# Optimization experiments

Measured on AMD Instinct MI355X. Metric: run time of the kernel, lower is better.

Reference implementation:

```python
import jax, jax.numpy as jnp
import numpy as np

B, H, N, D = 64, 12, 196, 768  # ViT-B/16 @ 224: 196 patch tokens + 1 CLS


def setup_inputs() -> dict:
    key = jax.random.key(0)
    k1, k2, k3 = jax.random.split(key, 3)
    student_tokens = jax.random.normal(k1, (B, N, D), dtype=jnp.float32)
    teacher_tokens = jax.random.normal(k2, (B, N, D), dtype=jnp.float32)
    teacher_attn = jax.random.uniform(k3, (B, H, N + 1, N + 1), dtype=jnp.float32)
    return {
        "student_tokens": student_tokens,
        "teacher_tokens": teacher_tokens,
        "teacher_attn": teacher_attn,
    }


def reference(student_tokens, teacher_tokens, teacher_attn):
    s = student_tokens.astype(jnp.float32)
    t = teacher_tokens.astype(jnp.float32)
    # CLS->patch attention, averaged over heads: [B, N]
    w = teacher_attn[:, :, 0, 1:].mean(axis=1)
    w = w / (w.sum(axis=-1, keepdims=True) + 1e-8)
    s = w[..., None] * s
    t = w[..., None] * t
    # center over token dim
    s_c = s - s.mean(axis=1, keepdims=True)
    t_c = t - t.mean(axis=1, keepdims=True)
    tr_s = jnp.sum(s_c * s_c, axis=(1, 2))  # [B]
    tr_t = jnp.sum(t_c * t_c, axis=(1, 2))  # [B]
    # cross-covariance: [B, D, D]
    cross = jnp.einsum("bnd,bne->bde", s_c, t_c)
    # nuclear norm = sum of singular values
    nuclear = jnp.linalg.svd(cross, compute_uv=False).sum(axis=-1)  # [B]
    loss = jnp.maximum(tr_s + tr_t - 2.0 * nuclear, 0.0).mean()
    return loss
```

## Files before the change

### kernel.cpp

```cpp
#include <hip/hip_runtime.h>
#include <hip/hip_bf16.h>
#include <math.h>

#define NTOK 196
#define NDIM 768
#define NB 64
#define NH 12
#define NA 197
#define MAT (NTOK * NTOK)
#define ATTN_HW (NA * NA)
#define POLAR_ITERS 15

#define PADC 208
#define NTILE 13
#define POLAR_LDS_BYTES (2 * NTOK * PADC * 2)

#define GCH 64
#define GPLANE (208 * GCH)
#define GRAM_LDS_BYTES (2 * GPLANE * 2)

#define FCH 64
#define FA_ROWS 208
#define FB_ROWS 112
#define FAPLANE (FA_ROWS * FCH)
#define FBPLANE (FB_ROWS * FCH)
#define FMF_LDS_BYTES ((2 * FAPLANE + 2 * FBPLANE) * 2)

#define HCH 64
#define HPLANE (208 * HCH)
#define H_LDS_BYTES (2 * HPLANE * 2)
#define NS_SCR_BYTES (8 * 16 * 17 * 4)
#define NS_LDS_BYTES (FMF_LDS_BYTES + NS_SCR_BYTES)

#define POW_LD 197
#define POW_F_WORDS (NTOK * POW_LD)
#define POW_LDS_BYTES ((POW_F_WORDS + 2 * NTOK + 256) * 4)

#define PTLD 208
#define TRI_WORDS 19306
#define CHOL2_PT_WORDS (16 * PTLD)
#define CHOL2_TRI_OFF CHOL2_PT_WORDS
#define CHOL2_ROWOFF_OFF (CHOL2_TRI_OFF + TRI_WORDS)
#define CHOL2_PV_OFF 22832
#define CHOL2_LDS_BYTES ((CHOL2_PV_OFF + 32) * 4)

typedef __attribute__((ext_vector_type(8))) short short8;
typedef __attribute__((ext_vector_type(4))) short short4_t;
typedef __attribute__((ext_vector_type(4))) float f32x4;

__device__ inline short8 s8zero() { short8 z = {0,0,0,0,0,0,0,0}; return z; }

__device__ inline short f2bf(float f) {
  union { float f; unsigned u; } v; v.f = f;
  unsigned u = v.u;
  u += 0x7fffu + ((u >> 16) & 1u);
  return (short)(u >> 16);
}
__device__ inline float bf2f(short s) {
  union { unsigned u; float f; } v;
  v.u = ((unsigned)(unsigned short)s) << 16;
  return v.f;
}

__global__ void k_w(const float* __restrict__ attn, float* __restrict__ wbuf) {
  int b = blockIdx.x;
  int tid = threadIdx.x;
  __shared__ float red[256];
  float w0 = 0.f;
  if (tid < NTOK) {
    size_t base = (size_t)b * NH * ATTN_HW + 1 + tid;
    #pragma unroll
    for (int h = 0; h < NH; ++h) w0 += attn[base + (size_t)h * ATTN_HW];
    w0 *= (1.f / NH);
  }
  red[tid] = (tid < NTOK) ? w0 : 0.f;
  __syncthreads();
  for (int s = 128; s > 0; s >>= 1) { if (tid < s) red[tid] += red[tid + s]; __syncthreads(); }
  float S = red[0];
  if (tid < NTOK) wbuf[b * NTOK + tid] = w0 / (S + 1e-8f);
}

__global__ __launch_bounds__(512, 1) void k_gram_mfma(
    const float* __restrict__ s, const float* __restrict__ t,
    const float* __restrict__ wbuf, float* __restrict__ Gbuf) {
  extern __shared__ short gsm[];
  short* bhp = gsm;
  short* blp = gsm + GPLANE;
  __shared__ float wsh[NTOK];
  int slot = blockIdx.x, b = slot >> 1, src = slot & 1;
  const float* X = (src ? t : s) + (size_t)b * NTOK * NDIM;
  int tid = threadIdx.x;
  int wave = tid >> 6, ln15 = tid & 15, quad = (tid >> 4) & 3;

  if (tid < NTOK) wsh[tid] = wbuf[b * NTOK + tid];
  for (int i = tid; i < 768; i += 512) {
    int p = i / 384, o = i - p * 384;
    ((int*)(gsm + p * GPLANE + 196 * GCH))[o] = 0;
  }
  __syncthreads();

  f32x4 zz = {0.f, 0.f, 0.f, 0.f};
  f32x4 acc[12];
  #pragma unroll
  for (int j = 0; j < 12; ++j) acc[j] = zz;

  for (int c = 0; c < NDIM / GCH; ++c) {
    int kc = c * GCH;
    for (int gi = tid; gi < NTOK * 8; gi += 512) {
      int r = gi >> 3, g = gi & 7;
      const float* sp = X + (size_t)r * NDIM + kc + g * 8;
      float4 f0 = *(const float4*)(sp);
      float4 f1 = *(const float4*)(sp + 4);
      float wv = wsh[r];
      float vs[8] = {f0.x, f0.y, f0.z, f0.w, f1.x, f1.y, f1.z, f1.w};
      short8 hv, lv;
      #pragma unroll
      for (int e = 0; e < 8; ++e) {
        float y = wv * vs[e];
        short hb = f2bf(y);
        hv[e] = hb;
        lv[e] = f2bf(y - bf2f(hb));
      }
      int pg = (g ^ (r & 7)) * 8;
      *(short8*)(bhp + r * GCH + pg) = hv;
      *(short8*)(blp + r * GCH + pg) = lv;
    }
    __syncthreads();
    #pragma unroll
    for (int j = 0; j < 12; ++j) {
      int T = wave + 8 * j;
      if (T < 91) {
        int ti = (int)((sqrtf(8.f * T + 1.f) - 1.f) * 0.5f);
        if ((ti + 1) * (ti + 2) / 2 <= T) ++ti;
        if (ti * (ti + 1) / 2 > T) --ti;
        int tj = T - ti * (ti + 1) / 2;
        int ra = ti * 16 + ln15, rb = tj * 16 + ln15;
        #pragma unroll
        for (int ks = 0; ks < 2; ++ks) {
          int gb0 = ks * 4 + quad;
          int ga = (gb0 ^ (ra & 7)) * 8, gb = (gb0 ^ (rb & 7)) * 8;
          short8 ah = *(const short8*)(bhp + ra * GCH + ga);
          short8 al = *(const short8*)(blp + ra * GCH + ga);
          short8 bhf = *(const short8*)(bhp + rb * GCH + gb);
          short8 blf = *(const short8*)(blp + rb * GCH + gb);
          acc[j] = __builtin_amdgcn_mfma_f32_16x16x32_bf16(ah, bhf, acc[j], 0, 0, 0);
          acc[j] = __builtin_amdgcn_mfma_f32_16x16x32_bf16(ah, blf, acc[j], 0, 0, 0);
          acc[j] = __builtin_amdgcn_mfma_f32_16x16x32_bf16(al, bhf, acc[j], 0, 0, 0);
        }
      }
    }
    __syncthreads();
  }

  float* G = Gbuf + (size_t)slot * MAT;
  #pragma unroll
  for (int j = 0; j < 12; ++j) {
    int T = wave + 8 * j;
    if (T < 91) {
      int ti = (int)((sqrtf(8.f * T + 1.f) - 1.f) * 0.5f);
      if ((ti + 1) * (ti + 2) / 2 <= T) ++ti;
      if (ti * (ti + 1) / 2 > T) --ti;
      int tj = T - ti * (ti + 1) / 2;
      int col = tj * 16 + ln15;
      #pragma unroll
      for (int r = 0; r < 4; ++r) {
        int row = ti * 16 + quad * 4 + r;
        if (row < NTOK && col < NTOK) {
          G[row * NTOK + col] = acc[j][r];
          if (ti != tj) G[col * NTOK + row] = acc[j][r];
        }
      }
    }
  }
}

__global__ void k_center(float* __restrict__ Gbuf, float* __restrict__ trPb) {
  int slot = blockIdx.x;
  float* A = Gbuf + (size_t)slot * MAT;
  __shared__ float r[NTOK];
  __shared__ float red[256];
  __shared__ float gsh, dsh;
  int tid = threadIdx.x;
  float acc = 0.f;
  if (tid < NTOK) {
    for (int m = 0; m < NTOK; ++m) acc += A[m * NTOK + tid];
    r[tid] = acc * (1.f / NTOK);
  }
  red[tid] = (tid < NTOK) ? acc * (1.f / NTOK) : 0.f;
  __syncthreads();
  for (int s = 128; s > 0; s >>= 1) { if (tid < s) red[tid] += red[tid + s]; __syncthreads(); }
  float g = red[0] * (1.f / NTOK);
  float tv = (tid < NTOK) ? (A[tid * NTOK + tid] - 2.f * r[tid] + g) : 0.f;
  __syncthreads();
  red[tid] = tv;
  __syncthreads();
  for (int s = 128; s > 0; s >>= 1) { if (tid < s) red[tid] += red[tid + s]; __syncthreads(); }
  if (tid == 0) {
    float tr = red[0];
    trPb[slot] = tr;
    gsh = g;
    dsh = 1e-4f * fmaxf(tr, 0.f) * (1.f / NTOK);
  }
  __syncthreads();
  float gg = gsh, dd = dsh;
  for (int idx = tid; idx < MAT; idx += 256) {
    int n = idx / NTOK, m = idx - n * NTOK;
    float v = A[idx] - r[n] - r[m] + gg;
    if (n == m) v += dd;
    A[idx] = v;
  }
}

__global__ __launch_bounds__(256, 1) void k_chol_panel(float* __restrict__ Gbuf,
                                                       int transposeOut) {
  extern __shared__ float smf[];
  float* Pt = smf;
  float* tri = smf + CHOL2_TRI_OFF;
  int* rowoff = (int*)(smf + CHOL2_ROWOFF_OFF);
  float* pvb = smf + CHOL2_PV_OFF;
  int slot = blockIdx.x;
  float* A = Gbuf + (size_t)slot * MAT;
  int tid = threadIdx.x;
  if (tid < NTOK) rowoff[tid] = tid * (tid + 1) / 2;
  __syncthreads();
  for (int idx = tid; idx < MAT; idx += 256) {
    int i = idx / NTOK, j = idx - i * NTOK;
    if (j <= i) tri[rowoff[i] + j] = A[idx];
  }
  __syncthreads();

  for (int k0 = 0; k0 < NTOK; k0 += 16) {
    int nb = (NTOK - k0 < 16) ? (NTOK - k0) : 16;
    int t = tid;
    int i = k0 + t;
    bool hasrow = (t < NTOK - k0);
    int ro = hasrow ? rowoff[i] : 0;

    float a[16];
    #pragma unroll
    for (int jj = 0; jj < 16; ++jj) a[jj] = 0.f;
    if (hasrow) {
      #pragma unroll
      for (int jj = 0; jj < 16; ++jj)
        if (jj < nb && k0 + jj <= i) a[jj] = tri[ro + k0 + jj];
    }

    #pragma unroll
    for (int jj = 0; jj < 16; ++jj) {
      bool cv = (jj < nb);
      if (cv && hasrow && t >= jj && t < nb) pvb[((jj & 1) << 4) + t] = a[jj];
      __syncthreads();
      if (cv && hasrow && t >= jj) {
        const float* pv = pvb + ((jj & 1) << 4);
        f32x4 p0 = *(const f32x4*)(pv);
        f32x4 p1 = *(const f32x4*)(pv + 4);
        f32x4 p2 = *(const f32x4*)(pv + 8);
        f32x4 p3 = *(const f32x4*)(pv + 12);
        float pvj = (jj < 4) ? p0[jj & 3] : (jj < 8) ? p1[jj & 3]
                   : (jj < 12) ? p2[jj & 3] : p3[jj & 3];
        float sq = sqrtf(fmaxf(pvj, 1e-20f));
        float pivinv = 1.f / sq;
        float v = a[jj] * pivinv;
        a[jj] = v;
        #pragma unroll
        for (int m = 0; m < 16; ++m) {
          if (m > jj) {
            float pvm = (m < 4) ? p0[m & 3] : (m < 8) ? p1[m & 3]
                       : (m < 12) ? p2[m & 3] : p3[m & 3];
            if (m < nb) a[m] -= v * (pvm * pivinv);
          }
        }
      }
    }

    if (hasrow) {
      #pragma unroll
      for (int jj = 0; jj < 16; ++jj)
        if (jj < nb && k0 + jj <= i) tri[ro + k0 + jj] = a[jj];
      if (t >= nb) {
        #pragma unroll
        for (int jj = 0; jj < 16; ++jj)
          if (jj < nb) Pt[jj * PTLD + i] = a[jj];
      }
    }
    __syncthreads();

    int k1 = k0 + nb;
    int nrem = NTOK - k1;
    if (nrem > 0) {
      int ntile = (nrem + 3) >> 2;
      int Ttot = ntile * (ntile + 1) / 2;
      for (int T = tid; T < Ttot; T += 256) {
        float disc = (2.f * ntile + 1.f) * (2.f * ntile + 1.f) - 8.f * (float)T;
        int tm = (int)((2.f * ntile + 1.f - sqrtf(fmaxf(disc, 0.f))) * 0.5f);
        if (tm > ntile - 1) tm = ntile - 1;
        if (tm < 0) tm = 0;
        #define FCOL(c) ((c) * ntile - (((c) * ((c) - 1)) >> 1))
        while (tm + 1 <= ntile - 1 && FCOL(tm + 1) <= T) ++tm;
        while (tm > 0 && FCOL(tm) > T) --tm;
        int ti = tm + (T - FCOL(tm));
        #undef FCOL
        int i0 = k1 + ti * 4, m0 = k1 + tm * 4;
        f32x4 acc0 = {0.f, 0.f, 0.f, 0.f};
        f32x4 acc1 = acc0, acc2 = acc0, acc3 = acc0;
        #pragma unroll
        for (int jj = 0; jj < 16; ++jj) {
          if (jj < nb) {
            f32x4 li = *(const f32x4*)(Pt + jj * PTLD + i0);
            f32x4 lm = *(const f32x4*)(Pt + jj * PTLD + m0);
            acc0 += lm * li[0];
            acc1 += lm * li[1];
            acc2 += lm * li[2];
            acc3 += lm * li[3];
          }
        }
        #define STORE_ROW(r, av)                                        \
          { int ii = i0 + (r);                                          \
            if (ii < NTOK) {                                            \
              int roi = rowoff[ii];                                     \
              if (m0 + 0 <= ii) tri[roi + m0 + 0] -= (av)[0];           \
              if (m0 + 1 <= ii) tri[roi + m0 + 1] -= (av)[1];           \
              if (m0 + 2 <= ii) tri[roi + m0 + 2] -= (av)[2];           \
              if (m0 + 3 <= ii) tri[roi + m0 + 3] -= (av)[3];           \
            } }
        STORE_ROW(0, acc0)
        STORE_ROW(1, acc1)
        STORE_ROW(2, acc2)
        STORE_ROW(3, acc3)
        #undef STORE_ROW
      }
    }
    __syncthreads();
  }

  if (transposeOut) {
    for (int idx = tid; idx < MAT; idx += 256) {
      int r2 = idx / NTOK, c2 = idx - r2 * NTOK;
      A[idx] = (r2 <= c2) ? tri[rowoff[c2] + r2] : 0.f;
    }
  } else {
    for (int idx = tid; idx < MAT; idx += 256) {
      int i = idx / NTOK, j = idx - i * NTOK;
      A[idx] = (j <= i) ? tri[rowoff[i] + j] : 0.f;
    }
  }
}

__global__ void k_chol_global(float* __restrict__ Gbuf) {
  int slot = blockIdx.x;
  float* A = Gbuf + (size_t)slot * MAT;
  __shared__ float col[NTOK];
  __shared__ float piv;
  int tid = threadIdx.x;
  for (int k = 0; k < NTOK; ++k) {
    if (tid == 0) { float p = sqrtf(fmaxf(A[k * NTOK + k], 1e-20f)); A[k * NTOK + k] = p; piv = p; }
    __syncthreads();
    float inv = 1.f / piv;
    for (int i = k + 1 + tid; i < NTOK; i += 256) {
      float v = A[i * NTOK + k] * inv;
      A[i * NTOK + k] = v;
      col[i] = v;
    }
    for (int j = k + 1 + tid; j < NTOK; j += 256) A[k * NTOK + j] = 0.f;
    __syncthreads();
    int nrem = NTOK - 1 - k;
    int total = nrem * (nrem + 1) / 2;
    for (int tt = tid; tt < total; tt += 256) {
      int a = (int)((sqrtf(8.f * tt + 1.f) - 1.f) * 0.5f);
      while ((a + 1) * (a + 2) / 2 <= tt) ++a;
      while (a * (a + 1) / 2 > tt) --a;
      int bb = tt - a * (a + 1) / 2;
      int i = k + 1 + a, j = k + 1 + bb;
      A[i * NTOK + j] -= col[i] * col[j];
    }
    __syncthreads();
  }
}

__global__ __launch_bounds__(512, 1) void k_F_mfma(const float* __restrict__ Gbuf,
                                                   float* __restrict__ Fbuf) {
  extern __shared__ short fsm[];
  short* Ah = fsm;
  short* Al = Ah + FAPLANE;
  short* Bh = Al + FAPLANE;
  short* Bl = Bh + FBPLANE;
  int half = blockIdx.x, b = blockIdx.y;
  const float* LTp = Gbuf + (size_t)(2 * b) * MAT;
  const float* LTq = Gbuf + (size_t)(2 * b + 1) * MAT;
  int co = half * 112;
  int tid = threadIdx.x;
  int wave = tid >> 6, ln15 = tid & 15, quad = (tid >> 4) & 3;

  f32x4 zz = {0.f, 0.f, 0.f, 0.f};
  f32x4 acc[12];
  #pragma unroll
  for (int j = 0; j < 12; ++j) acc[j] = zz;

  for (int c = 0; c < 4; ++c) {
    int kc = c * FCH;
    bool fullchunk = (kc + FCH <= NTOK);
    for (int gi = tid; gi < (FA_ROWS + FB_ROWS) * 8; gi += 512) {
      bool isA = gi < FA_ROWS * 8;
      int li = isA ? gi : gi - FA_ROWS * 8;
      int r = li >> 3, g = li & 7;
      int grow = isA ? r : co + r;
      short8 hv = s8zero(), lv = s8zero();
      if (grow < NTOK) {
        const float* src = (isA ? LTp : LTq) + (size_t)grow * NTOK + kc + g * 8;
        if (fullchunk) {
          float4 f0 = *(const float4*)(src);
          float4 f1 = *(const float4*)(src + 4);
          float vs[8] = {f0.x, f0.y, f0.z, f0.w, f1.x, f1.y, f1.z, f1.w};
          #pragma unroll
          for (int e = 0; e < 8; ++e) {
            short hb = f2bf(vs[e]);
            hv[e] = hb;
            lv[e] = f2bf(vs[e] - bf2f(hb));
          }
        } else {
          #pragma unroll
          for (int e = 0; e < 8; ++e) {
            int k = kc + g * 8 + e;
            if (k < NTOK) {
              float y = src[e];
              short hb = f2bf(y);
              hv[e] = hb;
              lv[e] = f2bf(y - bf2f(hb));
            }
          }
        }
      }
      int pg = (g ^ (r & 7)) * 8;
      if (isA) {
        *(short8*)(Ah + r * FCH + pg) = hv;
        *(short8*)(Al + r * FCH + pg) = lv;
      } else {
        *(short8*)(Bh + r * FCH + pg) = hv;
        *(short8*)(Bl + r * FCH + pg) = lv;
      }
    }
    __syncthreads();
    #pragma unroll
    for (int j = 0; j < 12; ++j) {
      int T = wave + 8 * j;
      if (T < 91) {
        int ti = T / 7, tj = T - ti * 7;
        if (co + tj * 16 < NTOK) {
          int ra = ti * 16 + ln15;
          int rb = tj * 16 + ln15;
          #pragma unroll
          for (int ks = 0; ks < 2; ++ks) {
            int gb0 = ks * 4 + quad;
            int ga = (gb0 ^ (ra & 7)) * 8, gb = (gb0 ^ (rb & 7)) * 8;
            short8 ah = *(const short8*)(Ah + ra * FCH + ga);
            short8 al = *(const short8*)(Al + ra * FCH + ga);
            short8 bh = *(const short8*)(Bh + rb * FCH + gb);
            short8 bl = *(const short8*)(Bl + rb * FCH + gb);
            acc[j] = __builtin_amdgcn_mfma_f32_16x16x32_bf16(ah, bh, acc[j], 0, 0, 0);
            acc[j] = __builtin_amdgcn_mfma_f32_16x16x32_bf16(ah, bl, acc[j], 0, 0, 0);
            acc[j] = __builtin_amdgcn_mfma_f32_16x16x32_bf16(al, bh, acc[j], 0, 0, 0);
          }
        }
      }
    }
    __syncthreads();
  }

  float* F = Fbuf + (size_t)b * MAT;
  #pragma unroll
  for (int j = 0; j < 12; ++j) {
    int T = wave + 8 * j;
    if (T < 91) {
      int ti = T / 7, tj = T - ti * 7;
      int col = co + tj * 16 + ln15;
      if (col < NTOK) {
        #pragma unroll
        for (int r = 0; r < 4; ++r) {
          int row = ti * 16 + quad * 4 + r;
          if (row < NTOK) F[row * NTOK + col] = acc[j][r];
        }
      }
    }
  }
}

__global__ void k_F(const float* __restrict__ Gbuf, float* __restrict__ Fbuf) {
  int b = blockIdx.y;
  const float* Lp = Gbuf + (size_t)(2 * b) * MAT;
  const float* Lq = Gbuf + (size_t)(2 * b + 1) * MAT;
  int ti = blockIdx.x / 7, tj = blockIdx.x % 7;
  int ri = ti * 32, cj = tj * 32;
  __shared__ float As[32][33], Bs[32][33];
  int tid = threadIdx.x, ty = tid >> 4, tx = tid & 15;
  float a00 = 0, a01 = 0, a10 = 0, a11 = 0;
  for (int k0 = 0; k0 < NTOK; k0 += 32) {
    for (int l = tid; l < 1024; l += 256) {
      int kk = l >> 5, ii = l & 31;
      int krow = k0 + kk;
      As[kk][ii] = (krow < NTOK && ri + ii < NTOK) ? Lp[(size_t)krow * NTOK + ri + ii] : 0.f;
      Bs[kk][ii] = (krow < NTOK && cj + ii < NTOK) ? Lq[(size_t)krow * NTOK + cj + ii] : 0.f;
    }
    __syncthreads();
    #pragma unroll
    for (int kk = 0; kk < 32; ++kk) {
      float p0 = As[kk][ty], p1 = As[kk][ty + 16];
      float q0 = Bs[kk][tx], q1 = Bs[kk][tx + 16];
      a00 += p0 * q0; a01 += p0 * q1; a10 += p1 * q0; a11 += p1 * q1;
    }
    __syncthreads();
  }
  float* F = Fbuf + (size_t)b * MAT;
  int i0 = ri + ty, i1 = ri + ty + 16, j0 = cj + tx, j1 = cj + tx + 16;
  if (i0 < NTOK && j0 < NTOK) F[i0 * NTOK + j0] = a00;
  if (i0 < NTOK && j1 < NTOK) F[i0 * NTOK + j1] = a01;
  if (i1 < NTOK && j0 < NTOK) F[i1 * NTOK + j0] = a10;
  if (i1 < NTOK && j1 < NTOK) F[i1 * NTOK + j1] = a11;
}

__global__ __launch_bounds__(256, 1) void k_pow_lds(const float* __restrict__ Fbuf,
                                                    float* __restrict__ nrmb) {
  extern __shared__ float psm[];
  float* Fsh = psm;
  float* v = psm + POW_F_WORDS;
  float* u = v + NTOK;
  float* red = u + NTOK;
  int b = blockIdx.x;
  const float* F = Fbuf + (size_t)b * MAT;
  int tid = threadIdx.x;
  for (int idx = tid; idx < MAT; idx += 256) {
    int i = idx / NTOK, j = idx - i * NTOK;
    Fsh[i * POW_LD + j] = F[idx];
  }
  if (tid < NTOK) v[tid] = 1.f;
  __syncthreads();
  float lastsum = 1.f;
  for (int it = 0; it < 6; ++it) {
    if (tid < NTOK) {
      float a = 0.f;
      for (int j = 0; j < NTOK; ++j) a += Fsh[tid * POW_LD + j] * v[j];
      u[tid] = a;
    }
    __syncthreads();
    float a2 = 0.f;
    if (tid < NTOK) { for (int i = 0; i < NTOK; ++i) a2 += Fsh[i * POW_LD + tid] * u[i]; }
    red[tid] = (tid < NTOK) ? a2 * a2 : 0.f;
    __syncthreads();
    for (int s2 = 128; s2 > 0; s2 >>= 1) { if (tid < s2) red[tid] += red[tid + s2]; __syncthreads(); }
    float sum = red[0];
    lastsum = sum;
    float invn = rsqrtf(sum + 1e-30f);
    __syncthreads();
    if (tid < NTOK) v[tid] = a2 * invn;
    __syncthreads();
  }
  if (tid == 0) {
    float sig = sqrtf(sqrtf(lastsum));
    nrmb[b] = 1.f / (1.1f * sig + 1e-30f);
  }
}

__global__ void k_pow(const float* __restrict__ Fbuf, float* __restrict__ nrmb) {
  int b = blockIdx.x;
  const float* F = Fbuf + (size_t)b * MAT;
  __shared__ float v[NTOK], u[NTOK];
  __shared__ float red[256];
  int tid = threadIdx.x;
  if (tid < NTOK) v[tid] = 1.f;
  __syncthreads();
  float lastsum = 1.f;
  for (int it = 0; it < 6; ++it) {
    float a = 0.f;
    if (tid < NTOK) { for (int j = 0; j < NTOK; ++j) a += F[tid * NTOK + j] * v[j]; }
    __syncthreads();
    if (tid < NTOK) u[tid] = a;
    __syncthreads();
    float a2 = 0.f;
    if (tid < NTOK) { for (int i = 0; i < NTOK; ++i) a2 += F[i * NTOK + tid] * u[i]; }
    red[tid] = (tid < NTOK) ? a2 * a2 : 0.f;
    __syncthreads();
    for (int s = 128; s > 0; s >>= 1) { if (tid < s) red[tid] += red[tid + s]; __syncthreads(); }
    float sum = red[0];
    lastsum = sum;
    float invn = rsqrtf(sum + 1e-30f);
    __syncthreads();
    if (tid < NTOK) v[tid] = a2 * invn;
    __syncthreads();
  }
  if (tid == 0) {
    float sig = sqrtf(sqrtf(lastsum));
    nrmb[b] = 1.f / (1.1f * sig + 1e-30f);
  }
}

__global__ void k_scale(const float* __restrict__ Fbuf, const float* __restrict__ nrmb,
                        float* __restrict__ X) {
  int b = blockIdx.y;
  int idx = blockIdx.x * 256 + threadIdx.x;
  if (idx < MAT) X[(size_t)b * MAT + idx] = Fbuf[(size_t)b * MAT + idx] * nrmb[b];
}

__global__ __launch_bounds__(512, 1) void k_polar_fused(
    const float* __restrict__ Fbuf, const float* __restrict__ nrmb,
    float* __restrict__ Xout) {
  extern __shared__ short sm[];
  short* bufA = sm;
  short* bufB = sm + NTOK * PADC;
  int b = blockIdx.x;
  const float* F = Fbuf + (size_t)b * MAT;
  float* XO = Xout + (size_t)b * MAT;
  int tid = threadIdx.x;
  int wave = tid >> 6, ln15 = tid & 15, quad = (tid >> 4) & 3;
  int rt0 = wave, rt1 = wave + 8;
  bool has2 = (rt1 < NTILE);

  for (int i = tid; i < (2 * NTOK * PADC) / 2; i += 512) ((int*)sm)[i] = 0;
  __syncthreads();
  float invc = nrmb[b];
  for (int idx = tid; idx < MAT; idx += 512) {
    int i = idx / NTOK, j = idx - i * NTOK;
    bufA[i * PADC + j] = f2bf(F[idx] * invc);
  }
  __syncthreads();

  int arow0 = rt0 * 16 + ln15;
  int arow1 = rt1 * 16 + ln15;
  bool av1 = has2 && (arow1 < NTOK);
  int m0a = rt0 * 16 + quad * 4;
  int m1a = rt1 * 16 + quad * 4;

  for (int it = 0; it < POLAR_ITERS; ++it) {
    {
      short8 a0[7], a1[7];
      #pragma unroll
      for (int ks = 0; ks < 7; ++ks) {
        int kk = ks * 32 + quad * 8;
        a0[ks] = (kk < PADC) ? *(const short8*)(bufA + arow0 * PADC + kk) : s8zero();
        a1[ks] = (av1 && kk < PADC) ? *(const short8*)(bufA + arow1 * PADC + kk) : s8zero();
      }
      for (int ct = 0; ct < NTILE; ++ct) {
        int brow = ct * 16 + ln15;
        bool bv = brow < NTOK;
        f32x4 acc0 = {0.f, 0.f, 0.f, 0.f};
        f32x4 acc1 = {0.f, 0.f, 0.f, 0.f};
        #pragma unroll
        for (int ks = 0; ks < 7; ++ks) {
          int kk = ks * 32 + quad * 8;
          short8 bfr = (bv && kk < PADC) ? *(const short8*)(bufA + brow * PADC + kk) : s8zero();
          acc0 = __builtin_amdgcn_mfma_f32_16x16x32_bf16(a0[ks], bfr, acc0, 0, 0, 0);
          if (has2)
            acc1 = __builtin_amdgcn_mfma_f32_16x16x32_bf16(a1[ks], bfr, acc1, 0, 0, 0);
        }
        if (bv) {
          short4_t w0;
          #pragma unroll
          for (int r = 0; r < 4; ++r) {
            float h = -0.5f * acc0[r] + ((m0a + r == brow) ? 1.5f : 0.f);
            w0[r] = f2bf(h);
          }
          *(short4_t*)(bufB + brow * PADC + m0a) = w0;
          if (has2) {
            short4_t w1;
            #pragma unroll
            for (int r = 0; r < 4; ++r) {
              float h = -0.5f * acc1[r] + ((m1a + r == brow) ? 1.5f : 0.f);
              w1[r] = f2bf(h);
            }
            *(short4_t*)(bufB + brow * PADC + m1a) = w1;
          }
        }
      }
    }
    __syncthreads();
    {
      short8 g0[7], g1[7];
      #pragma unroll
      for (int ks = 0; ks < 7; ++ks) {
        int kk = ks * 32 + quad * 8;
        short8 v0 = s8zero(), v1 = s8zero();
        if (kk < PADC) {
          #pragma unroll
          for (int j = 0; j < 8; ++j) {
            v0[j] = bufA[(kk + j) * PADC + arow0];
            if (has2) v1[j] = bufA[(kk + j) * PADC + arow1];
          }
        }
        g0[ks] = v0; g1[ks] = v1;
      }
      __syncthreads();
      for (int ct = 0; ct < NTILE; ++ct) {
        int n = ct * 16 + ln15;
        bool nv = n < NTOK;
        f32x4 acc0 = {0.f, 0.f, 0.f, 0.f};
        f32x4 acc1 = {0.f, 0.f, 0.f, 0.f};
        #pragma unroll
        for (int ks = 0; ks < 7; ++ks) {
          int kk = ks * 32 + quad * 8;
          short8 bfr = (nv && kk < PADC) ? *(const short8*)(bufB + n * PADC + kk) : s8zero();
          acc0 = __builtin_amdgcn_mfma_f32_16x16x32_bf16(g0[ks], bfr, acc0, 0, 0, 0);
          if (has2)
            acc1 = __builtin_amdgcn_mfma_f32_16x16x32_bf16(g1[ks], bfr, acc1, 0, 0, 0);
        }
        if (nv) {
          short4_t w0;
          #pragma unroll
          for (int r = 0; r < 4; ++r) w0[r] = f2bf(acc0[r]);
          *(short4_t*)(bufA + n * PADC + m0a) = w0;
          if (has2) {
            short4_t w1;
            #pragma unroll
            for (int r = 0; r < 4; ++r) w1[r] = f2bf(acc1[r]);
            *(short4_t*)(bufA + n * PADC + m1a) = w1;
          }
        }
      }
    }
    __syncthreads();
  }

  for (int idx = tid; idx < MAT; idx += 512) {
    int i = idx / NTOK, j = idx - i * NTOK;
    XO[idx] = bf2f(bufA[i * PADC + j]);
  }
}

__global__ void k_transpose(const float* __restrict__ Xb, float* __restrict__ Xt) {
  int b = blockIdx.y;
  int ti = blockIdx.x / 7, tj = blockIdx.x % 7;
  const float* X = Xb + (size_t)b * MAT;
  float* T = Xt + (size_t)b * MAT;
  __shared__ float ts[32][33];
  int tid = threadIdx.x;
  int r = tid >> 5, c = tid & 31;
  for (int rr = r; rr < 32; rr += 8) {
    int gi = ti * 32 + rr, gj = tj * 32 + c;
    ts[rr][c] = (gi < NTOK && gj < NTOK) ? X[gi * NTOK + gj] : 0.f;
  }
  __syncthreads();
  for (int rr = r; rr < 32; rr += 8) {
    int go = tj * 32 + rr, gc = ti * 32 + c;
    if (go < NTOK && gc < NTOK) T[go * NTOK + gc] = ts[c][rr];
  }
}

__global__ __launch_bounds__(512, 1) void k_h_mfma(const float* __restrict__ Xb,
                                                   float* __restrict__ Hb) {
  extern __shared__ short hsm[];
  short* bhp = hsm;
  short* blp = hsm + HPLANE;
  int b = blockIdx.x;
  const float* X = Xb + (size_t)b * MAT;
  int tid = threadIdx.x;
  int wave = tid >> 6, ln15 = tid & 15, quad = (tid >> 4) & 3;

  for (int i = tid; i < 768; i += 512) {
    int p = i / 384, o = i - p * 384;
    ((int*)(hsm + p * HPLANE + 196 * HCH))[o] = 0;
  }
  __syncthreads();

  f32x4 zz = {0.f, 0.f, 0.f, 0.f};
  f32x4 acc[12];
  #pragma unroll
  for (int j = 0; j < 12; ++j) acc[j] = zz;

  for (int c = 0; c < 4; ++c) {
    int kc = c * HCH;
    bool full = (kc + HCH <= NTOK);
    for (int gi = tid; gi < NTOK * 8; gi += 512) {
      int r = gi >> 3, g = gi & 7;
      const float* sp = X + (size_t)r * NTOK + kc + g * 8;
      short8 hv = s8zero(), lv = s8zero();
      if (full) {
        float4 f0 = *(const float4*)(sp);
        float4 f1 = *(const float4*)(sp + 4);
        float vs[8] = {f0.x, f0.y, f0.z, f0.w, f1.x, f1.y, f1.z, f1.w};
        #pragma unroll
        for (int e = 0; e < 8; ++e) {
          short hb = f2bf(vs[e]);
          hv[e] = hb;
          lv[e] = f2bf(vs[e] - bf2f(hb));
        }
      } else {
        #pragma unroll
        for (int e = 0; e < 8; ++e) {
          int k = kc + g * 8 + e;
          if (k < NTOK) {
            float y = sp[e];
            short hb = f2bf(y);
            hv[e] = hb;
            lv[e] = f2bf(y - bf2f(hb));
          }
        }
      }
      int pg = (g ^ (r & 7)) * 8;
      *(short8*)(bhp + r * HCH + pg) = hv;
      *(short8*)(blp + r * HCH + pg) = lv;
    }
    __syncthreads();
    #pragma unroll
    for (int j = 0; j < 12; ++j) {
      int T = wave + 8 * j;
      if (T < 91) {
        int ti = (int)((sqrtf(8.f * T + 1.f) - 1.f) * 0.5f);
        if ((ti + 1) * (ti + 2) / 2 <= T) ++ti;
        if (ti * (ti + 1) / 2 > T) --ti;
        int tj = T - ti * (ti + 1) / 2;
        int ra = ti * 16 + ln15, rb = tj * 16 + ln15;
        #pragma unroll
        for (int ks = 0; ks < 2; ++ks) {
          int gb0 = ks * 4 + quad;
          int ga = (gb0 ^ (ra & 7)) * 8, gb = (gb0 ^ (rb & 7)) * 8;
          short8 ah = *(const short8*)(bhp + ra * HCH + ga);
          short8 al = *(const short8*)(blp + ra * HCH + ga);
          short8 bhf = *(const short8*)(bhp + rb * HCH + gb);
          short8 blf = *(const short8*)(blp + rb * HCH + gb);
          acc[j] = __builtin_amdgcn_mfma_f32_16x16x32_bf16(ah, bhf, acc[j], 0, 0, 0);
          acc[j] = __builtin_amdgcn_mfma_f32_16x16x32_bf16(ah, blf, acc[j], 0, 0, 0);
          acc[j] = __builtin_amdgcn_mfma_f32_16x16x32_bf16(al, bhf, acc[j], 0, 0, 0);
        }
      }
    }
    __syncthreads();
  }

  float* H = Hb + (size_t)b * MAT;
  #pragma unroll
  for (int j = 0; j < 12; ++j) {
    int T = wave + 8 * j;
    if (T < 91) {
      int ti = (int)((sqrtf(8.f * T + 1.f) - 1.f) * 0.5f);
      if ((ti + 1) * (ti + 2) / 2 <= T) ++ti;
      if (ti * (ti + 1) / 2 > T) --ti;
      int tj = T - ti * (ti + 1) / 2;
      int col = tj * 16 + ln15;
      #pragma unroll
      for (int r = 0; r < 4; ++r) {
        int row = ti * 16 + quad * 4 + r;
        if (row < NTOK && col < NTOK) {
          H[row * NTOK + col] = acc[j][r];
          if (ti != tj) H[col * NTOK + row] = acc[j][r];
        }
      }
    }
  }
}

__global__ __launch_bounds__(512, 1) void k_nsup_mfma(
    const float* __restrict__ Hb, const float* __restrict__ Wb,
    const float* __restrict__ Xb, float* __restrict__ Xn,
    float* __restrict__ Wn, int writeW) {
  extern __shared__ short nsm[];
  short* Ah = nsm;
  short* Al = Ah + FAPLANE;
  short* Bh = Al + FAPLANE;
  short* Bl = Bh + FBPLANE;
  float* scr = (float*)(nsm + 2 * FAPLANE + 2 * FBPLANE);
  int half = blockIdx.x, b = blockIdx.y;
  const float* H = Hb + (size_t)b * MAT;
  const float* W = Wb + (size_t)b * MAT;
  const float* X = Xb + (size_t)b * MAT;
  int co = half * 112;
  int tid = threadIdx.x;
  int wave = tid >> 6, ln15 = tid & 15, quad = (tid >> 4) & 3;

  f32x4 zz = {0.f, 0.f, 0.f, 0.f};
  f32x4 acc[12];
  #pragma unroll
  for (int j = 0; j < 12; ++j) acc[j] = zz;

  for (int c = 0; c < 4; ++c) {
    int kc = c * FCH;
    bool fullchunk = (kc + FCH <= NTOK);
    for (int gi = tid; gi < (FA_ROWS + FB_ROWS) * 8; gi += 512) {
      bool isA = gi < FA_ROWS * 8;
      int li = isA ? gi : gi - FA_ROWS * 8;
      int r = li >> 3, g = li & 7;
      int grow = isA ? r : co + r;
      short8 hv = s8zero(), lv = s8zero();
      if (grow < NTOK) {
        const float* src = (isA ? H : W) + (size_t)grow * NTOK + kc + g * 8;
        if (fullchunk) {
          float4 f0 = *(const float4*)(src);
          float4 f1 = *(const float4*)(src + 4);
          float vs[8] = {f0.x, f0.y, f0.z, f0.w, f1.x, f1.y, f1.z, f1.w};
          #pragma unroll
          for (int e = 0; e < 8; ++e) {
            short hb = f2bf(vs[e]);
            hv[e] = hb;
            lv[e] = f2bf(vs[e] - bf2f(hb));
          }
        } else {
          #pragma unroll
          for (int e = 0; e < 8; ++e) {
            int k = kc + g * 8 + e;
            if (k < NTOK) {
              float y = src[e];
              short hb = f2bf(y);
              hv[e] = hb;
              lv[e] = f2bf(y - bf2f(hb));
            }
          }
        }
      }
      int pg = (g ^ (r & 7)) * 8;
      if (isA) {
        *(short8*)(Ah + r * FCH + pg) = hv;
        *(short8*)(Al + r * FCH + pg) = lv;
      } else {
        *(short8*)(Bh + r * FCH + pg) = hv;
        *(short8*)(Bl + r * FCH + pg) = lv;
      }
    }
    __syncthreads();
    #pragma unroll
    for (int j = 0; j < 12; ++j) {
      int T = wave + 8 * j;
      if (T < 91) {
        int ti = T / 7, tj = T - ti * 7;
        if (co + tj * 16 < NTOK) {
          int ra = ti * 16 + ln15;
          int rb = tj * 16 + ln15;
          #pragma unroll
          for (int ks = 0; ks < 2; ++ks) {
            int gb0 = ks * 4 + quad;
            int ga = (gb0 ^ (ra & 7)) * 8, gb = (gb0 ^ (rb & 7)) * 8;
            short8 ah = *(const short8*)(Ah + ra * FCH + ga);
            short8 al = *(const short8*)(Al + ra * FCH + ga);
            short8 bh = *(const short8*)(Bh + rb * FCH + gb);
            short8 bl = *(const short8*)(Bl + rb * FCH + gb);
            acc[j] = __builtin_amdgcn_mfma_f32_16x16x32_bf16(ah, bh, acc[j], 0, 0, 0);
            acc[j] = __builtin_amdgcn_mfma_f32_16x16x32_bf16(ah, bl, acc[j], 0, 0, 0);
            acc[j] = __builtin_amdgcn_mfma_f32_16x16x32_bf16(al, bh, acc[j], 0, 0, 0);
          }
        }
      }
    }
    __syncthreads();
  }

  float* XnB = Xn + (size_t)b * MAT;
  float* WnB = writeW ? (Wn + (size_t)b * MAT) : (float*)0;
  float* ws = scr + wave * 16 * 17;
  #pragma unroll
  for (int j = 0; j < 12; ++j) {
    int T = wave + 8 * j;
    if (T < 91) {
      int ti = T / 7, tj = T - ti * 7;
      int colbase = co + tj * 16;
      if (colbase < NTOK) {
        int col = colbase + ln15;
        float vr[4];
        #pragma unroll
        for (int r = 0; r < 4; ++r) {
          int row = ti * 16 + quad * 4 + r;
          bool valid = (row < NTOK) && (col < NTOK);
          float v = valid ? (1.5f * X[row * NTOK + col] - 0.5f * acc[j][r]) : 0.f;
          vr[r] = v;
          if (valid) XnB[row * NTOK + col] = v;
        }
        if (writeW) {
          #pragma unroll
          for (int r = 0; r < 4; ++r) ws[ln15 * 17 + quad * 4 + r] = vr[r];
          #pragma unroll
          for (int rr = 0; rr < 4; ++rr) {
            int ro = colbase + quad * 4 + rr;
            int cc = ti * 16 + ln15;
            if (ro < NTOK && cc < NTOK)
              WnB[ro * NTOK + cc] = ws[(quad * 4 + rr) * 17 + ln15];
          }
        }
      }
    }
  }
}

__global__ void k_xtx(const float* __restrict__ Xb, float* __restrict__ Gp) {
  int b = blockIdx.y;
  const float* X = Xb + (size_t)b * MAT;
  int x = blockIdx.x, ti = 0;
  while (x >= ti + 1) { x -= ti + 1; ++ti; }
  int tj = x;
  int ri = ti * 32, cj = tj * 32;
  __shared__ float As[32][33], Bs[32][33];
  int tid = threadIdx.x, ty = tid >> 4, tx = tid & 15;
  float a00 = 0, a01 = 0, a10 = 0, a11 = 0;
  for (int k0 = 0; k0 < NTOK; k0 += 32) {
    for (int l = tid; l < 1024; l += 256) {
      int kk = l >> 5, ii = l & 31;
      int krow = k0 + kk;
      As[kk][ii] = (krow < NTOK && ri + ii < NTOK) ? X[(size_t)krow * NTOK + ri + ii] : 0.f;
      Bs[kk][ii] = (krow < NTOK && cj + ii < NTOK) ? X[(size_t)krow * NTOK + cj + ii] : 0.f;
    }
    __syncthreads();
    #pragma unroll
    for (int kk = 0; kk < 32; ++kk) {
      float p0 = As[kk][ty], p1 = As[kk][ty + 16];
      float q0 = Bs[kk][tx], q1 = Bs[kk][tx + 16];
      a00 += p0 * q0; a01 += p0 * q1; a10 += p1 * q0; a11 += p1 * q1;
    }
    __syncthreads();
  }
  float* G = Gp + (size_t)b * MAT;
  int i0 = ri + ty, i1 = ri + ty + 16, j0 = cj + tx, j1 = cj + tx + 16;
  if (i0 < NTOK && j0 < NTOK) { G[i0 * NTOK + j0] = a00; G[j0 * NTOK + i0] = a00; }
  if (i0 < NTOK && j1 < NTOK) { G[i0 * NTOK + j1] = a01; G[j1 * NTOK + i0] = a01; }
  if (i1 < NTOK && j0 < NTOK) { G[i1 * NTOK + j0] = a10; G[j0 * NTOK + i1] = a10; }
  if (i1 < NTOK && j1 < NTOK) { G[i1 * NTOK + j1] = a11; G[j1 * NTOK + i1] = a11; }
}

__global__ void k_nsup(const float* __restrict__ Xb, const float* __restrict__ Gp,
                       float* __restrict__ Xn) {
  int b = blockIdx.y;
  const float* X = Xb + (size_t)b * MAT;
  const float* G = Gp + (size_t)b * MAT;
  int ti = blockIdx.x / 7, tj = blockIdx.x % 7;
  int ri = ti * 32, cj = tj * 32;
  __shared__ float As[32][33], Bs[32][33];
  int tid = threadIdx.x, ty = tid >> 4, tx = tid & 15;
  float a00 = 0, a01 = 0, a10 = 0, a11 = 0;
  for (int k0 = 0; k0 < NTOK; k0 += 32) {
    for (int l = tid; l < 1024; l += 256) {
      int rr = l >> 5, cc = l & 31;
      As[rr][cc] = (ri + rr < NTOK && k0 + cc < NTOK) ? X[(size_t)(ri + rr) * NTOK + k0 + cc] : 0.f;
      Bs[rr][cc] = (k0 + rr < NTOK && cj + cc < NTOK) ? G[(size_t)(k0 + rr) * NTOK + cj + cc] : 0.f;
    }
    __syncthreads();
    #pragma unroll
    for (int kk = 0; kk < 32; ++kk) {
      float p0 = As[ty][kk], p1 = As[ty + 16][kk];
      float q0 = Bs[kk][tx], q1 = Bs[kk][tx + 16];
      a00 += p0 * q0; a01 += p0 * q1; a10 += p1 * q0; a11 += p1 * q1;
    }
    __syncthreads();
  }
  float* O = Xn + (size_t)b * MAT;
  int i0 = ri + ty, i1 = ri + ty + 16, j0 = cj + tx, j1 = cj + tx + 16;
  if (i0 < NTOK && j0 < NTOK) O[i0 * NTOK + j0] = 1.5f * X[i0 * NTOK + j0] - 0.5f * a00;
  if (i0 < NTOK && j1 < NTOK) O[i0 * NTOK + j1] = 1.5f * X[i0 * NTOK + j1] - 0.5f * a01;
  if (i1 < NTOK && j0 < NTOK) O[i1 * NTOK + j0] = 1.5f * X[i1 * NTOK + j0] - 0.5f * a10;
  if (i1 < NTOK && j1 < NTOK) O[i1 * NTOK + j1] = 1.5f * X[i1 * NTOK + j1] - 0.5f * a11;
}

__global__ void k_nuc(const float* __restrict__ U, const float* __restrict__ Fbuf,
                      float* __restrict__ nucb) {
  int b = blockIdx.x;
  int tid = threadIdx.x;
  const float* Ub = U + (size_t)b * MAT;
  const float* Fb = Fbuf + (size_t)b * MAT;
  float acc = 0.f;
  for (int idx = tid; idx < MAT; idx += 256) acc += Ub[idx] * Fb[idx];
  __shared__ float red[256];
  red[tid] = acc;
  __syncthreads();
  for (int s = 128; s > 0; s >>= 1) { if (tid < s) red[tid] += red[tid + s]; __syncthreads(); }
  if (tid == 0) nucb[b] = red[0];
}

__global__ void k_final(const float* __restrict__ trPb, const float* __restrict__ nucb,
                        float* __restrict__ out) {
  int tid = threadIdx.x;
  float v = fmaxf(trPb[2 * tid] + trPb[2 * tid + 1] - 2.f * nucb[tid], 0.f);
  #pragma unroll
  for (int off = 32; off; off >>= 1) v += __shfl_down(v, off);
  if (tid == 0) out[0] = v * (1.f / 64.f);
}

extern "C" void kernel_launch(void* const* d_in, const int* in_sizes, int n_in,
                              void* d_out, int out_size, void* d_ws, size_t ws_size,
                              hipStream_t stream) {
  (void)in_sizes; (void)n_in; (void)out_size; (void)ws_size;
  const float* s = (const float*)d_in[0];
  const float* t = (const float*)d_in[1];
  const float* attn = (const float*)d_in[2];
  float* out = (float*)d_out;

  float* W = (float*)d_ws;
  float* Gbuf = W;
  float* Fbuf = Gbuf + (size_t)128 * MAT;
  float* Xbuf = Fbuf + (size_t)64 * MAT;
  float* Xnew = Xbuf + (size_t)64 * MAT;
  float* Gpol = Xnew + (size_t)64 * MAT;
  float* Xt0  = Gpol + (size_t)64 * MAT;
  float* Xt1  = Xt0 + (size_t)64 * MAT;
  float* wbuf = Xt1 + (size_t)64 * MAT;
  float* trPb = wbuf + (size_t)NB * NTOK;
  float* nucb = trPb + 128;
  float* nrmb = nucb + 64;

  k_w<<<NB, 256, 0, stream>>>(attn, wbuf);
  k_gram_mfma<<<128, 512, GRAM_LDS_BYTES, stream>>>(s, t, wbuf, Gbuf);
  k_center<<<128, 256, 0, stream>>>(Gbuf, trPb);

  hipError_t chol_ok = hipFuncSetAttribute(
      reinterpret_cast<const void*>(k_chol_panel),
      hipFuncAttributeMaxDynamicSharedMemorySize, CHOL2_LDS_BYTES);
  hipError_t fmf_ok = hipFuncSetAttribute(
      reinterpret_cast<const void*>(k_F_mfma),
      hipFuncAttributeMaxDynamicSharedMemorySize, FMF_LDS_BYTES);
  bool mfmaF = (chol_ok == hipSuccess) && (fmf_ok == hipSuccess);

  if (chol_ok == hipSuccess) {
    k_chol_panel<<<128, 256, CHOL2_LDS_BYTES, stream>>>(Gbuf, mfmaF ? 1 : 0);
  } else {
    k_chol_global<<<128, 256, 0, stream>>>(Gbuf);
  }

  if (mfmaF) {
    k_F_mfma<<<dim3(2, 64), 512, FMF_LDS_BYTES, stream>>>(Gbuf, Fbuf);
  } else {
    k_F<<<dim3(49, 64), 256, 0, stream>>>(Gbuf, Fbuf);
  }

  hipError_t pow_ok = hipFuncSetAttribute(
      reinterpret_cast<const void*>(k_pow_lds),
      hipFuncAttributeMaxDynamicSharedMemorySize, POW_LDS_BYTES);
  if (pow_ok == hipSuccess) {
    k_pow_lds<<<64, 256, POW_LDS_BYTES, stream>>>(Fbuf, nrmb);
  } else {
    k_pow<<<64, 256, 0, stream>>>(Fbuf, nrmb);
  }

  hipError_t fused_ok = hipFuncSetAttribute(
      reinterpret_cast<const void*>(k_polar_fused),
      hipFuncAttributeMaxDynamicSharedMemorySize, POLAR_LDS_BYTES);
  hipError_t h_ok = hipFuncSetAttribute(
      reinterpret_cast<const void*>(k_h_mfma),
      hipFuncAttributeMaxDynamicSharedMemorySize, H_LDS_BYTES);
  hipError_t ns_ok = hipFuncSetAttribute(
      reinterpret_cast<const void*>(k_nsup_mfma),
      hipFuncAttributeMaxDynamicSharedMemorySize, NS_LDS_BYTES);
  bool mfmaPolish = (h_ok == hipSuccess) && (ns_ok == hipSuccess);

  const float* finalX;
  if (fused_ok == hipSuccess) {
    k_polar_fused<<<NB, 512, POLAR_LDS_BYTES, stream>>>(Fbuf, nrmb, Xbuf);
    if (mfmaPolish) {
      k_transpose<<<dim3(49, 64), 256, 0, stream>>>(Xbuf, Xt0);
      k_h_mfma<<<64, 512, H_LDS_BYTES, stream>>>(Xbuf, Gpol);
      k_nsup_mfma<<<dim3(2, 64), 512, NS_LDS_BYTES, stream>>>(Gpol, Xt0, Xbuf, Xnew, Xt1, 1);
      k_h_mfma<<<64, 512, H_LDS_BYTES, stream>>>(Xnew, Gpol);
      k_nsup_mfma<<<dim3(2, 64), 512, NS_LDS_BYTES, stream>>>(Gpol, Xt1, Xnew, Xbuf, (float*)0, 0);
    } else {
      k_xtx<<<dim3(28, 64), 256, 0, stream>>>(Xbuf, Gpol);
      k_nsup<<<dim3(49, 64), 256, 0, stream>>>(Xbuf, Gpol, Xnew);
      k_xtx<<<dim3(28, 64), 256, 0, stream>>>(Xnew, Gpol);
      k_nsup<<<dim3(49, 64), 256, 0, stream>>>(Xnew, Gpol, Xbuf);
    }
    finalX = Xbuf;
  } else {
    k_scale<<<dim3(151, 64), 256, 0, stream>>>(Fbuf, nrmb, Xbuf);
    float* Xc = Xbuf;
    float* Xn = Xnew;
    for (int it = 0; it < POLAR_ITERS; ++it) {
      k_xtx<<<dim3(28, 64), 256, 0, stream>>>(Xc, Gpol);
      k_nsup<<<dim3(49, 64), 256, 0, stream>>>(Xc, Gpol, Xn);
      float* tmp = Xc; Xc = Xn; Xn = tmp;
    }
    finalX = Xc;
  }

  k_nuc<<<64, 256, 0, stream>>>(finalX, Fbuf, nucb);
  k_final<<<1, 64, 0, stream>>>(trPb, nucb, out);
}
```

Before: 888.8 us.

## Fuse Gram centering into Gram kernel and split polish H-kernel across two blocks

Adds k_gramc, which computes the weighted Gram matrix with MFMA, stages it in LDS, and applies double-centering, trace and diagonal regularisation in place. This replaces the separate k_center pass and the global round-trip of the Gram matrix. Separately, k_h_mfma now splits the 91 upper-triangular tiles across two blocks per batch, so the launch grows from 64 to 128 blocks. The trade-off is a large LDS footprint that limits occupancy, plus duplicated operand staging in each half-block.

```diff
diff --git a/kernel.cpp b/kernel.cpp
--- a/kernel.cpp
+++ b/kernel.cpp
@@ -18,6 +18,8 @@
 #define GCH 64
 #define GPLANE (208 * GCH)
 #define GRAM_LDS_BYTES (2 * GPLANE * 2)
+#define GC_LD 200
+#define GC_LDS_BYTES (NTOK * GC_LD * 4)
 
 #define FCH 64
 #define FA_ROWS 208
@@ -78,6 +80,145 @@
   for (int s = 128; s > 0; s >>= 1) { if (tid < s) red[tid] += red[tid + s]; __syncthreads(); }
   float S = red[0];
   if (tid < NTOK) wbuf[b * NTOK + tid] = w0 / (S + 1e-8f);
+}
+
+__global__ __launch_bounds__(512, 1) void k_gramc(
+    const float* __restrict__ s, const float* __restrict__ t,
+    const float* __restrict__ wbuf, float* __restrict__ Gbuf,
+    float* __restrict__ trPb) {
+  extern __shared__ short gsm[];
+  short* bhp = gsm;
+  short* blp = gsm + GPLANE;
+  float* Gsh = (float*)gsm;
+  __shared__ float wsh[NTOK];
+  __shared__ float rr[NTOK];
+  __shared__ float red2[512];
+  __shared__ float gg_s, dd_s;
+  int slot = blockIdx.x, b = slot >> 1, src = slot & 1;
+  const float* X = (src ? t : s) + (size_t)b * NTOK * NDIM;
+  int tid = threadIdx.x;
+  int wave = tid >> 6, ln15 = tid & 15, quad = (tid >> 4) & 3;
+
+  if (tid < NTOK) wsh[tid] = wbuf[b * NTOK + tid];
+  for (int i = tid; i < 768; i += 512) {
+    int p = i / 384, o = i - p * 384;
+    ((int*)(gsm + p * GPLANE + 196 * GCH))[o] = 0;
+  }
+  __syncthreads();
+
+  f32x4 zz = {0.f, 0.f, 0.f, 0.f};
+  f32x4 acc[12];
+  #pragma unroll
+  for (int j = 0; j < 12; ++j) acc[j] = zz;
+
+  for (int c = 0; c < NDIM / GCH; ++c) {
+    int kc = c * GCH;
+    for (int gi = tid; gi < NTOK * 8; gi += 512) {
+      int r = gi >> 3, g = gi & 7;
+      const float* sp = X + (size_t)r * NDIM + kc + g * 8;
+      float4 f0 = *(const float4*)(sp);
+      float4 f1 = *(const float4*)(sp + 4);
+      float wv = wsh[r];
+      float vs[8] = {f0.x, f0.y, f0.z, f0.w, f1.x, f1.y, f1.z, f1.w};
+      short8 hv, lv;
+      #pragma unroll
+      for (int e = 0; e < 8; ++e) {
+        float y = wv * vs[e];
+        short hb = f2bf(y);
+        hv[e] = hb;
+        lv[e] = f2bf(y - bf2f(hb));
+      }
+      int pg = (g ^ (r & 7)) * 8;
+      *(short8*)(bhp + r * GCH + pg) = hv;
+      *(short8*)(blp + r * GCH + pg) = lv;
+    }
+    __syncthreads();
+    #pragma unroll
+    for (int j = 0; j < 12; ++j) {
+      int T = wave + 8 * j;
+      if (T < 91) {
+        int ti = (int)((sqrtf(8.f * T + 1.f) - 1.f) * 0.5f);
+        if ((ti + 1) * (ti + 2) / 2 <= T) ++ti;
+        if (ti * (ti + 1) / 2 > T) --ti;
+        int tj = T - ti * (ti + 1) / 2;
+        int ra = ti * 16 + ln15, rb = tj * 16 + ln15;
+        #pragma unroll
+        for (int ks = 0; ks < 2; ++ks) {
+          int gb0 = ks * 4 + quad;
+          int ga = (gb0 ^ (ra & 7)) * 8, gb = (gb0 ^ (rb & 7)) * 8;
+          short8 ah = *(const short8*)(bhp + ra * GCH + ga);
+          short8 al = *(const short8*)(blp + ra * GCH + ga);
+          short8 bhf = *(const short8*)(bhp + rb * GCH + gb);
+          short8 blf = *(const short8*)(blp + rb * GCH + gb);
+          acc[j] = __builtin_amdgcn_mfma_f32_16x16x32_bf16(ah, bhf, acc[j], 0, 0, 0);
+          acc[j] = __builtin_amdgcn_mfma_f32_16x16x32_bf16(ah, blf, acc[j], 0, 0, 0);
+          acc[j] = __builtin_amdgcn_mfma_f32_16x16x32_bf16(al, bhf, acc[j], 0, 0, 0);
+        }
+      }
+    }
+    __syncthreads();
+  }
+
+  #pragma unroll
+  for (int j = 0; j < 12; ++j) {
+    int T = wave + 8 * j;
+    if (T < 91) {
+      int ti = (int)((sqrtf(8.f * T + 1.f) - 1.f) * 0.5f);
+      if ((ti + 1) * (ti + 2) / 2 <= T) ++ti;
+      if (ti * (ti + 1) / 2 > T) --ti;
+      int tj = T - ti * (ti + 1) / 2;
+      int col = tj * 16 + ln15;
+      #pragma unroll
+      for (int r = 0; r < 4; ++r) {
+        int row = ti * 16 + quad * 4 + r;
+        if (row < NTOK && col < NTOK) {
+          Gsh[row * GC_LD + col] = acc[j][r];
+          if (ti != tj) Gsh[col * GC_LD + row] = acc[j][r];
+        }
+      }
+    }
+  }
+  __syncthreads();
+
+  float a0 = 0.f;
+  if (tid < NTOK) {
+    for (int m = 0; m < NTOK; ++m) a0 += Gsh[m * GC_LD + tid];
+    rr[tid] = a0 * (1.f / NTOK);
+  }
+  red2[tid] = (tid < NTOK) ? a0 * (1.f / NTOK) : 0.f;
+  __syncthreads();
+  for (int st = 256; st > 0; st >>= 1) { if (tid < st) red2[tid] += red2[tid + st]; __syncthreads(); }
+  float g = red2[0] * (1.f / NTOK);
+  float tv = (tid < NTOK) ? (Gsh[tid * GC_LD + tid] - 2.f * rr[tid] + g) : 0.f;
+  __syncthreads();
+  red2[tid] = tv;
+  __syncthreads();
+  for (int st = 256; st > 0; st >>= 1) { if (tid < st) red2[tid] += red2[tid + st]; __syncthreads(); }
+  if (tid == 0) {
+    float tr = red2[0];
+    trPb[slot] = tr;
+    gg_s = g;
+    dd_s = 1e-4f * fmaxf(tr, 0.f) * (1.f / NTOK);
+  }
+  __syncthreads();
+  float gv = gg_s, dv = dd_s;
+
+  float* G = Gbuf + (size_t)slot * MAT;
+  for (int q = tid; q < MAT / 4; q += 512) {
+    int idx = q * 4;
+    int n = idx / NTOK, m = idx - n * NTOK;
+    float rn = rr[n];
+    float v0 = Gsh[n * GC_LD + m + 0] - rn - rr[m + 0] + gv;
+    float v1 = Gsh[n * GC_LD + m + 1] - rn - rr[m + 1] + gv;
+    float v2 = Gsh[n * GC_LD + m + 2] - rn - rr[m + 2] + gv;
+    float v3 = Gsh[n * GC_LD + m + 3] - rn - rr[m + 3] + gv;
+    if (n == m) v0 += dv;
+    else if (n == m + 1) v1 += dv;
+    else if (n == m + 2) v2 += dv;
+    else if (n == m + 3) v3 += dv;
+    float4 o = {v0, v1, v2, v3};
+    ((float4*)G)[q] = o;
+  }
 }
 
 __global__ __launch_bounds__(512, 1) void k_gram_mfma(
@@ -747,7 +888,9 @@
   extern __shared__ short hsm[];
   short* bhp = hsm;
   short* blp = hsm + HPLANE;
-  int b = blockIdx.x;
+  int half = blockIdx.x, b = blockIdx.y;
+  int Tbase = half * 46;
+  int Tend = half ? 91 : 46;
   const float* X = Xb + (size_t)b * MAT;
   int tid = threadIdx.x;
   int wave = tid >> 6, ln15 = tid & 15, quad = (tid >> 4) & 3;
@@ -759,9 +902,9 @@
   __syncthreads();
 
   f32x4 zz = {0.f, 0.f, 0.f, 0.f};
-  f32x4 acc[12];
+  f32x4 acc[6];
   #pragma unroll
-  for (int j = 0; j < 12; ++j) acc[j] = zz;
+  for (int j = 0; j < 6; ++j) acc[j] = zz;
 
   for (int c = 0; c < 4; ++c) {
     int kc = c * HCH;
@@ -798,9 +941,9 @@
     }
     __syncthreads();
     #pragma unroll
-    for (int j = 0; j < 12; ++j) {
-      int T = wave + 8 * j;
-      if (T < 91) {
+    for (int j = 0; j < 6; ++j) {
+      int T = Tbase + wave + 8 * j;
+      if (T < Tend) {
         int ti = (int)((sqrtf(8.f * T + 1.f) - 1.f) * 0.5f);
         if ((ti + 1) * (ti + 2) / 2 <= T) ++ti;
         if (ti * (ti + 1) / 2 > T) --ti;
@@ -825,9 +968,9 @@
 
   float* H = Hb + (size_t)b * MAT;
   #pragma unroll
-  for (int j = 0; j < 12; ++j) {
-    int T = wave + 8 * j;
-    if (T < 91) {
+  for (int j = 0; j < 6; ++j) {
+    int T = Tbase + wave + 8 * j;
+    if (T < Tend) {
       int ti = (int)((sqrtf(8.f * T + 1.f) - 1.f) * 0.5f);
       if ((ti + 1) * (ti + 2) / 2 <= T) ++ti;
       if (ti * (ti + 1) / 2 > T) --ti;
@@ -1088,8 +1231,16 @@
   float* nrmb = nucb + 64;
 
   k_w<<<NB, 256, 0, stream>>>(attn, wbuf);
-  k_gram_mfma<<<128, 512, GRAM_LDS_BYTES, stream>>>(s, t, wbuf, Gbuf);
-  k_center<<<128, 256, 0, stream>>>(Gbuf, trPb);
+
+  hipError_t gc_ok = hipFuncSetAttribute(
+      reinterpret_cast<const void*>(k_gramc),
+      hipFuncAttributeMaxDynamicSharedMemorySize, GC_LDS_BYTES);
+  if (gc_ok == hipSuccess) {
+    k_gramc<<<128, 512, GC_LDS_BYTES, stream>>>(s, t, wbuf, Gbuf, trPb);
+  } else {
+    k_gram_mfma<<<128, 512, GRAM_LDS_BYTES, stream>>>(s, t, wbuf, Gbuf);
+    k_center<<<128, 256, 0, stream>>>(Gbuf, trPb);
+  }
 
   hipError_t chol_ok = hipFuncSetAttribute(
       reinterpret_cast<const void*>(k_chol_panel),
@@ -1136,9 +1287,9 @@
     k_polar_fused<<<NB, 512, POLAR_LDS_BYTES, stream>>>(Fbuf, nrmb, Xbuf);
     if (mfmaPolish) {
       k_transpose<<<dim3(49, 64), 256, 0, stream>>>(Xbuf, Xt0);
-      k_h_mfma<<<64, 512, H_LDS_BYTES, stream>>>(Xbuf, Gpol);
+      k_h_mfma<<<dim3(2, 64), 512, H_LDS_BYTES, stream>>>(Xbuf, Gpol);
       k_nsup_mfma<<<dim3(2, 64), 512, NS_LDS_BYTES, stream>>>(Gpol, Xt0, Xbuf, Xnew, Xt1, 1);
-      k_h_mfma<<<64, 512, H_LDS_BYTES, stream>>>(Xnew, Gpol);
+      k_h_mfma<<<dim3(2, 64), 512, H_LDS_BYTES, stream>>>(Xnew, Gpol);
       k_nsup_mfma<<<dim3(2, 64), 512, NS_LDS_BYTES, stream>>>(Gpol, Xt1, Xnew, Xbuf, (float*)0, 0);
     } else {
       k_xtx<<<dim3(28, 64), 256, 0, stream>>>(Xbuf, Gpol);
```

Result: slower. 1.092 ms (+22.9%).
